# Kernel tuning notes

Measured on AMD Instinct MI355X. Metric: run time of the kernel, lower is better.

The kernel has to match this reference:

```python
import jax, jax.numpy as jnp
import numpy as np

D_MODEL, D_FF, N_EXPERTS, TOP_K = 768, 3072, 8, 2
B, S = 2, 1024
LN_EPS = 1e-5


def setup_inputs() -> dict:
    key = jax.random.key(0)
    k1, k2, k3, k4 = jax.random.split(key, 4)
    return {
        "hidden_states": jax.random.normal(k1, (B, S, D_MODEL), dtype=jnp.float32),
        "ln_gamma": jnp.ones((D_MODEL,), dtype=jnp.float32),
        "ln_beta": jnp.zeros((D_MODEL,), dtype=jnp.float32),
        "router_w": jax.random.normal(k2, (D_MODEL, N_EXPERTS), dtype=jnp.float32) * 0.02,
        "w1": jax.random.normal(k3, (N_EXPERTS, D_MODEL, D_FF), dtype=jnp.float32) * 0.02,
        "w2": jax.random.normal(k4, (N_EXPERTS, D_FF, D_MODEL), dtype=jnp.float32) * 0.02,
    }


def _layernorm(x, gamma, beta):
    mu = jnp.mean(x, axis=-1, keepdims=True)
    var = jnp.mean(jnp.square(x - mu), axis=-1, keepdims=True)
    return (x - mu) * jax.lax.rsqrt(var + LN_EPS) * gamma + beta


def reference(hidden_states, ln_gamma, ln_beta, router_w, w1, w2):
    Bz, Sz, D = hidden_states.shape
    residual = hidden_states
    x = _layernorm(hidden_states, ln_gamma, ln_beta)
    tokens = x.reshape(-1, D)                       # [T, D]
    T = tokens.shape[0]

    # Router: softmax over experts, top-k selection, gate normalization
    logits = tokens @ router_w                      # [T, E]
    probs = jax.nn.softmax(logits, axis=-1)
    topw, topi = jax.lax.top_k(probs, TOP_K)        # [T, K]
    topw = topw / jnp.sum(topw, axis=-1, keepdims=True)  # normalize_gates=True

    # Dense gate matrix [T, E] (zero for unselected experts)
    gates = jnp.zeros((T, N_EXPERTS), dtype=tokens.dtype)
    gates = gates.at[jnp.arange(T)[:, None], topi].set(topw)

    # Per-expert FFN (silu, no bias), weighted combine
    h = jnp.einsum('td,edf->etf', tokens, w1)       # [E, T, F]
    h = jax.nn.silu(h)
    y = jnp.einsum('etf,efd->etd', h, w2)           # [E, T, D]
    out = jnp.einsum('te,etd->td', gates, y)        # [T, D]

    return residual + out.reshape(Bz, Sz, D)
```

## Files before the change

### kernel.cpp

```cpp
#include <hip/hip_runtime.h>
#include <hip/hip_bf16.h>
#include <math.h>

#define T_TOK 2048
#define DM 768
#define DF 3072
#define NE 8

typedef __attribute__((ext_vector_type(4))) float f32x4;
typedef __attribute__((ext_vector_type(8))) short bf16x8;

static __device__ __forceinline__ ushort f2bf(float f) {
    union { float f; unsigned u; } x; x.f = f;
    unsigned r = x.u + 0x7fff + ((x.u >> 16) & 1);
    return (ushort)(r >> 16);
}
static __device__ __forceinline__ float bf2f(ushort u) {
    union { unsigned u; float f; } x; x.u = ((unsigned)u) << 16; return x.f;
}
static __device__ __forceinline__ unsigned pk2(float lo, float hi) {
    return (unsigned)f2bf(lo) | ((unsigned)f2bf(hi) << 16);
}

__global__ __launch_bounds__(256) void ln_router_kernel(
    const float* __restrict__ hs, const float* __restrict__ gamma,
    const float* __restrict__ beta, const float* __restrict__ rw,
    ushort* __restrict__ xbf, float* __restrict__ topw, int* __restrict__ topi,
    int* __restrict__ counts)
{
    int t = blockIdx.x;
    int tid = threadIdx.x;
    const float* row = hs + (size_t)t * DM;
    float v[3];
    v[0] = row[tid]; v[1] = row[tid + 256]; v[2] = row[tid + 512];
    float s  = v[0] + v[1] + v[2];
    float sq = v[0]*v[0] + v[1]*v[1] + v[2]*v[2];
    #pragma unroll
    for (int off = 32; off > 0; off >>= 1) {
        s  += __shfl_down(s, off);
        sq += __shfl_down(sq, off);
    }
    __shared__ float wsum[4], wsq[4];
    __shared__ float pl[4][8];
    int lane = tid & 63, wv = tid >> 6;
    if (lane == 0) { wsum[wv] = s; wsq[wv] = sq; }
    __syncthreads();
    float tot  = wsum[0] + wsum[1] + wsum[2] + wsum[3];
    float totq = wsq[0] + wsq[1] + wsq[2] + wsq[3];
    float mu = tot * (1.0f / 768.0f);
    float var = totq * (1.0f / 768.0f) - mu * mu;
    float rstd = rsqrtf(var + 1e-5f);

    float p[8];
    #pragma unroll
    for (int e = 0; e < 8; e++) p[e] = 0.f;
    #pragma unroll
    for (int i = 0; i < 3; i++) {
        int d = tid + i * 256;
        float yv = (v[i] - mu) * rstd * gamma[d] + beta[d];
        xbf[(size_t)t * DM + d] = f2bf(yv);
        const float* r8 = rw + (size_t)d * 8;
        #pragma unroll
        for (int e = 0; e < 8; e++) p[e] += yv * r8[e];
    }
    #pragma unroll
    for (int off = 32; off > 0; off >>= 1) {
        #pragma unroll
        for (int e = 0; e < 8; e++) p[e] += __shfl_down(p[e], off);
    }
    if (lane == 0) {
        #pragma unroll
        for (int e = 0; e < 8; e++) pl[wv][e] = p[e];
    }
    __syncthreads();
    if (tid == 0) {
        float lg[8];
        #pragma unroll
        for (int e = 0; e < 8; e++) lg[e] = pl[0][e] + pl[1][e] + pl[2][e] + pl[3][e];
        int i0 = 0; float l0 = lg[0];
        #pragma unroll
        for (int e = 1; e < 8; e++) if (lg[e] > l0) { l0 = lg[e]; i0 = e; }
        int i1 = -1; float l1 = -3.4e38f;
        #pragma unroll
        for (int e = 0; e < 8; e++) if (e != i0 && lg[e] > l1) { l1 = lg[e]; i1 = e; }
        float w0 = 1.0f / (1.0f + __expf(l1 - l0));
        topi[2 * t] = i0;  topi[2 * t + 1] = i1;
        topw[2 * t] = w0;  topw[2 * t + 1] = 1.0f - w0;
        atomicAdd(&counts[i0], 1);
        atomicAdd(&counts[i1], 1);
    }
}

__global__ __launch_bounds__(256) void bucket_kernel(
    const int* __restrict__ topi, int* __restrict__ ctl,
    int* __restrict__ bucket_tok, int* __restrict__ tok_slot)
{
    int t = blockIdx.x * 256 + threadIdx.x;
    if (t >= T_TOK) return;
    int offs[8]; int acc = 0;
    #pragma unroll
    for (int e = 0; e < 8; e++) { offs[e] = acc; acc += ctl[e]; }
    #pragma unroll
    for (int k = 0; k < 2; k++) {
        int e = topi[2 * t + k];
        int pos = atomicAdd(&ctl[16 + e], 1);
        int idx = offs[e] + pos;
        bucket_tok[idx] = t;
        tok_slot[2 * t + k] = idx;
    }
}

__global__ __launch_bounds__(256) void wpack_kernel(
    const float* __restrict__ w1, const float* __restrict__ w2,
    unsigned* __restrict__ w1p, unsigned* __restrict__ w2p)
{
    const size_t MQ = (size_t)NE * DM * DF / 8;
    size_t stride = (size_t)gridDim.x * 256;
    for (size_t i = (size_t)blockIdx.x * 256 + threadIdx.x; i < 2 * MQ; i += stride) {
        bool m2 = i >= MQ;
        size_t o = (m2 ? i - MQ : i) * 4;
        int N = m2 ? DM : DF;
        size_t n = o % (size_t)N;
        const float* src = (m2 ? w2 : w1) + 2 * o - n;
        float4 a = *(const float4*)src;
        float4 b = *(const float4*)(src + N);
        uint4 r;
        r.x = pk2(a.x, b.x); r.y = pk2(a.y, b.y);
        r.z = pk2(a.z, b.z); r.w = pk2(a.w, b.w);
        *(uint4*)((m2 ? w2p : w1p) + o) = r;
    }
}

template<bool SILU, bool GATHER, int NT, int SPLITS>
__global__ __launch_bounds__(256) void moe_gemm(
    const ushort* __restrict__ A, const unsigned* __restrict__ Bp,
    ushort* __restrict__ C, const int* __restrict__ ctl,
    const int* __restrict__ bucket_tok, int K, int N)
{
    int bid = blockIdx.x;
    int e = bid & 7;
    int j = bid >> 3;
    int mt = j & 15;
    int c = j >> 4;
    int nt = c % NT;
    int sk = c / NT;
    int cnt = ctl[e];
    if (mt * 128 >= cnt) return;
    int off = 0;
    #pragma unroll
    for (int q = 0; q < 8; q++) if (q < e) off += ctl[q];
    const int Ks = K / SPLITS;
    int kbase = sk * Ks;

    __shared__ ushort Al[2][128 * 32];
    __shared__ unsigned Bl[2][16 * 128];

    int tid = threadIdx.x, lane = tid & 63, wv = tid >> 6;
    int kchunk = (lane & 3) * 8;

    const ushort* aptr[2];
    #pragma unroll
    for (int i = 0; i < 2; i++) {
        int r = i * 64 + wv * 16 + (lane >> 2);
        int gr = mt * 128 + r;
        if (gr >= cnt) gr = cnt - 1;
        if (GATHER) aptr[i] = A + (size_t)bucket_tok[off + gr] * K;
        else        aptr[i] = A + (size_t)(off + gr) * K;
    }
    const unsigned* Bb = Bp + (size_t)e * ((size_t)N * (K / 2));
    int n0 = nt * 128;
    int brow2[2], bscol[2];
    #pragma unroll
    for (int ii = 0; ii < 2; ii++) {
        int g = wv * 2 + ii;
        int row2 = 2 * g + (lane >> 5);
        int col4 = 4 * (lane & 31);
        brow2[ii] = row2;
        bscol[ii] = col4 ^ ((row2 & 7) << 2);
    }

    f32x4 acc[4][4];
    #pragma unroll
    for (int m = 0; m < 4; m++)
        #pragma unroll
        for (int n = 0; n < 4; n++)
            acc[m][n] = (f32x4){0.f, 0.f, 0.f, 0.f};

    int wr = wv >> 1, wc = wv & 1;
    int l15 = lane & 15, kq = lane >> 4;
    int ldstA = (wv * 16) * 32 + lane * 8;
    int xk = (kq & 1) << 4;

    auto stage = [&](int buf, int k0) {
        #pragma unroll
        for (int i = 0; i < 2; i++) {
            __builtin_amdgcn_global_load_lds(
                (const __attribute__((address_space(1))) void*)(aptr[i] + k0 + kchunk),
                (__attribute__((address_space(3))) void*)(&Al[buf][i * 64 * 32 + ldstA]),
                16, 0, 0);
        }
        int k2b = k0 >> 1;
        #pragma unroll
        for (int ii = 0; ii < 2; ii++) {
            int g = wv * 2 + ii;
            __builtin_amdgcn_global_load_lds(
                (const __attribute__((address_space(1))) void*)(Bb + (size_t)(k2b + brow2[ii]) * N + n0 + bscol[ii]),
                (__attribute__((address_space(3))) void*)(&Bl[buf][g * 256 + lane * 4]),
                16, 0, 0);
        }
    };

    const int nk = Ks >> 5;
    stage(0, kbase);
    asm volatile("s_waitcnt vmcnt(0)" ::: "memory");
    __builtin_amdgcn_s_barrier();

    for (int ks = 0; ks < nk; ks++) {
        int cur = ks & 1;
        if (ks + 1 < nk) stage(cur ^ 1, kbase + (ks + 1) * 32);
        bf16x8 af[4], bfr[4];
        #pragma unroll
        for (int m = 0; m < 4; m++)
            af[m] = *(const bf16x8*)&Al[cur][(wr * 64 + m * 16 + l15) * 32 + kq * 8];
        const unsigned* Blc = &Bl[cur][0];
        #pragma unroll
        for (int n = 0; n < 4; n++) {
            int ncol = wc * 64 + n * 16 + l15;
            union { uint4 u; bf16x8 h; } cvu;
            cvu.u.x = Blc[(kq * 4 + 0) * 128 + (ncol ^ (xk | 0))];
            cvu.u.y = Blc[(kq * 4 + 1) * 128 + (ncol ^ (xk | 4))];
            cvu.u.z = Blc[(kq * 4 + 2) * 128 + (ncol ^ (xk | 8))];
            cvu.u.w = Blc[(kq * 4 + 3) * 128 + (ncol ^ (xk | 12))];
            bfr[n] = cvu.h;
        }
        __builtin_amdgcn_s_setprio(1);
        #pragma unroll
        for (int m = 0; m < 4; m++)
            #pragma unroll
            for (int n = 0; n < 4; n++)
                acc[m][n] = __builtin_amdgcn_mfma_f32_16x16x32_bf16(af[m], bfr[n], acc[m][n], 0, 0, 0);
        __builtin_amdgcn_s_setprio(0);
        asm volatile("s_waitcnt vmcnt(0) lgkmcnt(0)" ::: "memory");
        __builtin_amdgcn_s_barrier();
    }

    #pragma unroll
    for (int m = 0; m < 4; m++) {
        #pragma unroll
        for (int n = 0; n < 4; n++) {
            #pragma unroll
            for (int jj = 0; jj < 4; jj++) {
                int gr = mt * 128 + wr * 64 + m * 16 + kq * 4 + jj;
                if (gr < cnt) {
                    float v = acc[m][n][jj];
                    if (SILU) v = v / (1.0f + __expf(-v));
                    int col = nt * 128 + wc * 64 + n * 16 + l15;
                    C[((size_t)sk * (T_TOK * 2) + off + gr) * N + col] = f2bf(v);
                }
            }
        }
    }
}

template<int SPLITS>
__global__ __launch_bounds__(256) void combine_kernel(
    const float* __restrict__ hs, const ushort* __restrict__ Yp,
    const float* __restrict__ topw, const int* __restrict__ tok_slot,
    float* __restrict__ out)
{
    int t = blockIdx.x, tid = threadIdx.x;
    int s0 = tok_slot[2 * t], s1 = tok_slot[2 * t + 1];
    float w0 = topw[2 * t], w1 = topw[2 * t + 1];
    const float* h = hs + (size_t)t * DM;
    float* o = out + (size_t)t * DM;
    #pragma unroll
    for (int i = 0; i < 3; i++) {
        int d = tid + i * 256;
        float y0 = 0.f, y1 = 0.f;
        #pragma unroll
        for (int s = 0; s < SPLITS; s++) {
            y0 += bf2f(Yp[((size_t)s * (T_TOK * 2) + s0) * DM + d]);
            y1 += bf2f(Yp[((size_t)s * (T_TOK * 2) + s1) * DM + d]);
        }
        o[d] = h[d] + w0 * y0 + w1 * y1;
    }
}

extern "C" void kernel_launch(void* const* d_in, const int* in_sizes, int n_in,
                              void* d_out, int out_size, void* d_ws, size_t ws_size,
                              hipStream_t stream)
{
    const float* hs    = (const float*)d_in[0];
    const float* gamma = (const float*)d_in[1];
    const float* beta  = (const float*)d_in[2];
    const float* rw    = (const float*)d_in[3];
    const float* w1    = (const float*)d_in[4];
    const float* w2    = (const float*)d_in[5];
    float* out = (float*)d_out;
    char* ws = (char*)d_ws;

    size_t o = 0;
    auto alc = [&](size_t b) { size_t r = o; o += (b + 255) & ~255ULL; return r; };
    int*      ctl        = (int*)(ws + alc(256));
    float*    topw       = (float*)(ws + alc((size_t)T_TOK * 2 * 4));
    int*      topi       = (int*)(ws + alc((size_t)T_TOK * 2 * 4));
    int*      tok_slot   = (int*)(ws + alc((size_t)T_TOK * 2 * 4));
    int*      bucket_tok = (int*)(ws + alc((size_t)T_TOK * 2 * 4));
    ushort*   xbf        = (ushort*)(ws + alc((size_t)T_TOK * DM * 2));
    unsigned* w1p        = (unsigned*)(ws + alc((size_t)NE * DF * DM * 2));
    unsigned* w2p        = (unsigned*)(ws + alc((size_t)NE * DF * DM * 2));
    ushort*   Hg         = (ushort*)(ws + alc((size_t)T_TOK * 2 * DF * 2));
    size_t yp_off        = alc((size_t)4 * T_TOK * 2 * DM * 2);
    ushort*   Yp         = (ushort*)(ws + yp_off);
    bool can_split       = (o <= ws_size);

    hipMemsetAsync(ctl, 0, 256, stream);
    wpack_kernel<<<2048, 256, 0, stream>>>(w1, w2, w1p, w2p);
    ln_router_kernel<<<T_TOK, 256, 0, stream>>>(hs, gamma, beta, rw, xbf, topw, topi, ctl);
    bucket_kernel<<<8, 256, 0, stream>>>(topi, ctl, bucket_tok, tok_slot);

    moe_gemm<true, true, 24, 1><<<8 * 16 * 24, 256, 0, stream>>>(
        xbf, w1p, Hg, ctl, bucket_tok, DM, DF);

    if (can_split) {
        moe_gemm<false, false, 6, 4><<<8 * 16 * 6 * 4, 256, 0, stream>>>(
            Hg, w2p, Yp, ctl, bucket_tok, DF, DM);
        combine_kernel<4><<<T_TOK, 256, 0, stream>>>(hs, Yp, topw, tok_slot, out);
    } else {
        moe_gemm<false, false, 6, 1><<<8 * 16 * 6, 256, 0, stream>>>(
            Hg, w2p, Yp, ctl, bucket_tok, DF, DM);
        combine_kernel<1><<<T_TOK, 256, 0, stream>>>(hs, Yp, topw, tok_slot, out);
    }
}
```

Baseline: 220.3 us.

## Fuse fp32-to-bf16 weight packing into GEMM B-tile staging

Removes the standalone weight-packing kernel and its packed bf16 workspace. The GEMMs now load fp32 weights into registers, convert and pair them into bf16, and write the swizzled layout to LDS themselves. This removes a full read-and-write pass over both weight tensors. In exchange, each m-tile reads fp32 weights (twice the bytes) and does conversion work in the inner loop, with a register round-trip instead of a direct-to-LDS load.

```diff
diff --git a/kernel.cpp b/kernel.cpp
--- a/kernel.cpp
+++ b/kernel.cpp
@@ -110,30 +110,9 @@
     }
 }
 
-__global__ __launch_bounds__(256) void wpack_kernel(
-    const float* __restrict__ w1, const float* __restrict__ w2,
-    unsigned* __restrict__ w1p, unsigned* __restrict__ w2p)
-{
-    const size_t MQ = (size_t)NE * DM * DF / 8;
-    size_t stride = (size_t)gridDim.x * 256;
-    for (size_t i = (size_t)blockIdx.x * 256 + threadIdx.x; i < 2 * MQ; i += stride) {
-        bool m2 = i >= MQ;
-        size_t o = (m2 ? i - MQ : i) * 4;
-        int N = m2 ? DM : DF;
-        size_t n = o % (size_t)N;
-        const float* src = (m2 ? w2 : w1) + 2 * o - n;
-        float4 a = *(const float4*)src;
-        float4 b = *(const float4*)(src + N);
-        uint4 r;
-        r.x = pk2(a.x, b.x); r.y = pk2(a.y, b.y);
-        r.z = pk2(a.z, b.z); r.w = pk2(a.w, b.w);
-        *(uint4*)((m2 ? w2p : w1p) + o) = r;
-    }
-}
-
 template<bool SILU, bool GATHER, int NT, int SPLITS>
 __global__ __launch_bounds__(256) void moe_gemm(
-    const ushort* __restrict__ A, const unsigned* __restrict__ Bp,
+    const ushort* __restrict__ A, const float* __restrict__ W,
     ushort* __restrict__ C, const int* __restrict__ ctl,
     const int* __restrict__ bucket_tok, int K, int N)
 {
@@ -167,16 +146,15 @@
         if (GATHER) aptr[i] = A + (size_t)bucket_tok[off + gr] * K;
         else        aptr[i] = A + (size_t)(off + gr) * K;
     }
-    const unsigned* Bb = Bp + (size_t)e * ((size_t)N * (K / 2));
+
+    const float* Wb = W + (size_t)e * ((size_t)K * N);
     int n0 = nt * 128;
-    int brow2[2], bscol[2];
+    int rp_[2], cc_[2];
     #pragma unroll
     for (int ii = 0; ii < 2; ii++) {
-        int g = wv * 2 + ii;
-        int row2 = 2 * g + (lane >> 5);
-        int col4 = 4 * (lane & 31);
-        brow2[ii] = row2;
-        bscol[ii] = col4 ^ ((row2 & 7) << 2);
+        int item = wv * 128 + ii * 64 + lane;
+        rp_[ii] = item >> 5;
+        cc_[ii] = item & 31;
     }
 
     f32x4 acc[4][4];
@@ -191,7 +169,9 @@
     int ldstA = (wv * 16) * 32 + lane * 8;
     int xk = (kq & 1) << 4;
 
-    auto stage = [&](int buf, int k0) {
+    float4 breg[2][2];
+
+    auto stageA = [&](int buf, int k0) {
         #pragma unroll
         for (int i = 0; i < 2; i++) {
             __builtin_amdgcn_global_load_lds(
@@ -199,25 +179,42 @@
                 (__attribute__((address_space(3))) void*)(&Al[buf][i * 64 * 32 + ldstA]),
                 16, 0, 0);
         }
-        int k2b = k0 >> 1;
+    };
+    auto bload = [&](int k0) {
         #pragma unroll
         for (int ii = 0; ii < 2; ii++) {
-            int g = wv * 2 + ii;
-            __builtin_amdgcn_global_load_lds(
-                (const __attribute__((address_space(1))) void*)(Bb + (size_t)(k2b + brow2[ii]) * N + n0 + bscol[ii]),
-                (__attribute__((address_space(3))) void*)(&Bl[buf][g * 256 + lane * 4]),
-                16, 0, 0);
+            const float* s = Wb + (size_t)(k0 + 2 * rp_[ii]) * N + n0 + 4 * cc_[ii];
+            breg[ii][0] = *(const float4*)s;
+            breg[ii][1] = *(const float4*)(s + N);
         }
     };
+    auto bwrite = [&](int buf) {
+        #pragma unroll
+        for (int ii = 0; ii < 2; ii++) {
+            uint4 r;
+            r.x = pk2(breg[ii][0].x, breg[ii][1].x);
+            r.y = pk2(breg[ii][0].y, breg[ii][1].y);
+            r.z = pk2(breg[ii][0].z, breg[ii][1].z);
+            r.w = pk2(breg[ii][0].w, breg[ii][1].w);
+            *(uint4*)&Bl[buf][rp_[ii] * 128 + ((4 * cc_[ii]) ^ ((rp_[ii] & 7) << 2))] = r;
+        }
+    };
 
     const int nk = Ks >> 5;
-    stage(0, kbase);
+    stageA(0, kbase);
+    bload(kbase);
     asm volatile("s_waitcnt vmcnt(0)" ::: "memory");
+    bwrite(0);
+    asm volatile("s_waitcnt lgkmcnt(0)" ::: "memory");
     __builtin_amdgcn_s_barrier();
 
     for (int ks = 0; ks < nk; ks++) {
         int cur = ks & 1;
-        if (ks + 1 < nk) stage(cur ^ 1, kbase + (ks + 1) * 32);
+        bool more = (ks + 1 < nk);
+        if (more) {
+            stageA(cur ^ 1, kbase + (ks + 1) * 32);
+            bload(kbase + (ks + 1) * 32);
+        }
         bf16x8 af[4], bfr[4];
         #pragma unroll
         for (int m = 0; m < 4; m++)
@@ -240,6 +237,10 @@
             for (int n = 0; n < 4; n++)
                 acc[m][n] = __builtin_amdgcn_mfma_f32_16x16x32_bf16(af[m], bfr[n], acc[m][n], 0, 0, 0);
         __builtin_amdgcn_s_setprio(0);
+        if (more) {
+            asm volatile("s_waitcnt vmcnt(0)" ::: "memory");
+            bwrite(cur ^ 1);
+        }
         asm volatile("s_waitcnt vmcnt(0) lgkmcnt(0)" ::: "memory");
         __builtin_amdgcn_s_barrier();
     }
@@ -307,28 +308,25 @@
     int*      tok_slot   = (int*)(ws + alc((size_t)T_TOK * 2 * 4));
     int*      bucket_tok = (int*)(ws + alc((size_t)T_TOK * 2 * 4));
     ushort*   xbf        = (ushort*)(ws + alc((size_t)T_TOK * DM * 2));
-    unsigned* w1p        = (unsigned*)(ws + alc((size_t)NE * DF * DM * 2));
-    unsigned* w2p        = (unsigned*)(ws + alc((size_t)NE * DF * DM * 2));
     ushort*   Hg         = (ushort*)(ws + alc((size_t)T_TOK * 2 * DF * 2));
     size_t yp_off        = alc((size_t)4 * T_TOK * 2 * DM * 2);
     ushort*   Yp         = (ushort*)(ws + yp_off);
     bool can_split       = (o <= ws_size);
 
     hipMemsetAsync(ctl, 0, 256, stream);
-    wpack_kernel<<<2048, 256, 0, stream>>>(w1, w2, w1p, w2p);
     ln_router_kernel<<<T_TOK, 256, 0, stream>>>(hs, gamma, beta, rw, xbf, topw, topi, ctl);
     bucket_kernel<<<8, 256, 0, stream>>>(topi, ctl, bucket_tok, tok_slot);
 
     moe_gemm<true, true, 24, 1><<<8 * 16 * 24, 256, 0, stream>>>(
-        xbf, w1p, Hg, ctl, bucket_tok, DM, DF);
+        xbf, w1, Hg, ctl, bucket_tok, DM, DF);
 
     if (can_split) {
         moe_gemm<false, false, 6, 4><<<8 * 16 * 6 * 4, 256, 0, stream>>>(
-            Hg, w2p, Yp, ctl, bucket_tok, DF, DM);
+            Hg, w2, Yp, ctl, bucket_tok, DF, DM);
         combine_kernel<4><<<T_TOK, 256, 0, stream>>>(hs, Yp, topw, tok_slot, out);
     } else {
         moe_gemm<false, false, 6, 1><<<8 * 16 * 6, 256, 0, stream>>>(
-            Hg, w2p, Yp, ctl, bucket_tok, DF, DM);
+            Hg, w2, Yp, ctl, bucket_tok, DF, DM);
         combine_kernel<1><<<T_TOK, 256, 0, stream>>>(hs, Yp, topw, tok_slot, out);
     }
 }
```

After: 212.3 us. -3.7%, faster.

## Triple-buffer MoE GEMM LDS pipeline, swizzle A tiles, split weight packing

Applied to the files above, without the earlier changes.

The expert GEMM moves from double to triple-buffered LDS staging. It waits with vmcnt(4) so one K-slice prefetch stays in flight during each compute step. The A tile layout in LDS gets an XOR swizzle on the K chunk to cut bank conflicts on fragment reads. Weight packing is split into two templated kernels with compile-time row length, uses the hardware v_cvt_pk_bf16_f32 conversion, and now launches after the router kernel. The cost is more LDS per block, which may lower occupancy, and an unrolled loop that assumes the K-step count is a multiple of three.

```diff
diff --git a/kernel.cpp b/kernel.cpp
--- a/kernel.cpp
+++ b/kernel.cpp
@@ -19,7 +19,9 @@
     union { unsigned u; float f; } x; x.u = ((unsigned)u) << 16; return x.f;
 }
 static __device__ __forceinline__ unsigned pk2(float lo, float hi) {
-    return (unsigned)f2bf(lo) | ((unsigned)f2bf(hi) << 16);
+    unsigned r;
+    asm("v_cvt_pk_bf16_f32 %0, %1, %2" : "=v"(r) : "v"(lo), "v"(hi));
+    return r;
 }
 
 __global__ __launch_bounds__(256) void ln_router_kernel(
@@ -110,24 +112,22 @@
     }
 }
 
+template<int N>
 __global__ __launch_bounds__(256) void wpack_kernel(
-    const float* __restrict__ w1, const float* __restrict__ w2,
-    unsigned* __restrict__ w1p, unsigned* __restrict__ w2p)
-{
-    const size_t MQ = (size_t)NE * DM * DF / 8;
-    size_t stride = (size_t)gridDim.x * 256;
-    for (size_t i = (size_t)blockIdx.x * 256 + threadIdx.x; i < 2 * MQ; i += stride) {
-        bool m2 = i >= MQ;
-        size_t o = (m2 ? i - MQ : i) * 4;
-        int N = m2 ? DM : DF;
-        size_t n = o % (size_t)N;
-        const float* src = (m2 ? w2 : w1) + 2 * o - n;
-        float4 a = *(const float4*)src;
-        float4 b = *(const float4*)(src + N);
+    const float* __restrict__ src, unsigned* __restrict__ dst, int total_q)
+{
+    int stride = gridDim.x * 256;
+    for (int i = blockIdx.x * 256 + threadIdx.x; i < total_q; i += stride) {
+        unsigned o = (unsigned)i * 4;
+        unsigned k2 = o / (unsigned)N;
+        unsigned n  = o - k2 * (unsigned)N;
+        const float* s = src + (size_t)(2 * k2) * N + n;
+        float4 a = *(const float4*)s;
+        float4 b = *(const float4*)(s + N);
         uint4 r;
         r.x = pk2(a.x, b.x); r.y = pk2(a.y, b.y);
         r.z = pk2(a.z, b.z); r.w = pk2(a.w, b.w);
-        *(uint4*)((m2 ? w2p : w1p) + o) = r;
+        *(uint4*)(dst + o) = r;
     }
 }
 
@@ -150,13 +150,13 @@
     #pragma unroll
     for (int q = 0; q < 8; q++) if (q < e) off += ctl[q];
     const int Ks = K / SPLITS;
-    int kbase = sk * Ks;
-
-    __shared__ ushort Al[2][128 * 32];
-    __shared__ unsigned Bl[2][16 * 128];
+    const int kbase = sk * Ks;
+
+    __shared__ ushort   Al[3][128 * 32];
+    __shared__ unsigned Bl[3][16 * 128];
 
     int tid = threadIdx.x, lane = tid & 63, wv = tid >> 6;
-    int kchunk = (lane & 3) * 8;
+    int kchA = ((lane & 3) ^ ((lane >> 3) & 3)) * 8;
 
     const ushort* aptr[2];
     #pragma unroll
@@ -195,7 +195,7 @@
         #pragma unroll
         for (int i = 0; i < 2; i++) {
             __builtin_amdgcn_global_load_lds(
-                (const __attribute__((address_space(1))) void*)(aptr[i] + k0 + kchunk),
+                (const __attribute__((address_space(1))) void*)(aptr[i] + k0 + kchA),
                 (__attribute__((address_space(3))) void*)(&Al[buf][i * 64 * 32 + ldstA]),
                 16, 0, 0);
         }
@@ -209,19 +209,13 @@
                 16, 0, 0);
         }
     };
-
-    const int nk = Ks >> 5;
-    stage(0, kbase);
-    asm volatile("s_waitcnt vmcnt(0)" ::: "memory");
-    __builtin_amdgcn_s_barrier();
-
-    for (int ks = 0; ks < nk; ks++) {
-        int cur = ks & 1;
-        if (ks + 1 < nk) stage(cur ^ 1, kbase + (ks + 1) * 32);
+    auto compute = [&](int cur) {
         bf16x8 af[4], bfr[4];
         #pragma unroll
-        for (int m = 0; m < 4; m++)
-            af[m] = *(const bf16x8*)&Al[cur][(wr * 64 + m * 16 + l15) * 32 + kq * 8];
+        for (int m = 0; m < 4; m++) {
+            int row = wr * 64 + m * 16 + l15;
+            af[m] = *(const bf16x8*)&Al[cur][row * 32 + ((kq ^ ((row >> 1) & 3)) << 3)];
+        }
         const unsigned* Blc = &Bl[cur][0];
         #pragma unroll
         for (int n = 0; n < 4; n++) {
@@ -240,9 +234,33 @@
             for (int n = 0; n < 4; n++)
                 acc[m][n] = __builtin_amdgcn_mfma_f32_16x16x32_bf16(af[m], bfr[n], acc[m][n], 0, 0, 0);
         __builtin_amdgcn_s_setprio(0);
-        asm volatile("s_waitcnt vmcnt(0) lgkmcnt(0)" ::: "memory");
-        __builtin_amdgcn_s_barrier();
-    }
+    };
+
+    const int nk = Ks >> 5;
+
+    stage(0, kbase);
+    stage(1, kbase + 32);
+    asm volatile("s_waitcnt vmcnt(4)" ::: "memory");
+    __builtin_amdgcn_s_barrier();
+
+    #define BODY(T, CUR, STG) { \
+        int t_ = (T); \
+        bool more2 = (t_ + 2 < nk); \
+        if (more2) stage(STG, kbase + (t_ + 2) * 32); \
+        compute(CUR); \
+        if (t_ + 1 < nk) { \
+            if (more2) asm volatile("s_waitcnt vmcnt(4)" ::: "memory"); \
+            else       asm volatile("s_waitcnt vmcnt(0)" ::: "memory"); \
+            __builtin_amdgcn_s_barrier(); \
+        } \
+    }
+
+    for (int t = 0; t < nk; t += 3) {
+        BODY(t,     0, 2);
+        BODY(t + 1, 1, 0);
+        BODY(t + 2, 2, 1);
+    }
+    #undef BODY
 
     #pragma unroll
     for (int m = 0; m < 4; m++) {
@@ -314,9 +332,12 @@
     ushort*   Yp         = (ushort*)(ws + yp_off);
     bool can_split       = (o <= ws_size);
 
+    const int WQ = NE * DM * DF / 8;
+
     hipMemsetAsync(ctl, 0, 256, stream);
-    wpack_kernel<<<2048, 256, 0, stream>>>(w1, w2, w1p, w2p);
     ln_router_kernel<<<T_TOK, 256, 0, stream>>>(hs, gamma, beta, rw, xbf, topw, topi, ctl);
+    wpack_kernel<DF><<<2048, 256, 0, stream>>>(w1, w1p, WQ);
+    wpack_kernel<DM><<<2048, 256, 0, stream>>>(w2, w2p, WQ);
     bucket_kernel<<<8, 256, 0, stream>>>(topi, ctl, bucket_tok, tok_slot);
 
     moe_gemm<true, true, 24, 1><<<8 * 16 * 24, 256, 0, stream>>>(
```

After: 268.4 us. +21.8%, slower.
